# Optimization experiments

Measured on AMD Instinct MI355X. Metric: run time of the kernel, lower is better.

The kernel has to match this reference:

```python
import jax, jax.numpy as jnp
import numpy as np

B, S, E, H, V, O = 64, 512, 128, 1024, 128, 128


def setup_inputs() -> dict:
    key = jax.random.key(0)
    ks = jax.random.split(key, 16)
    nrm = lambda k, shp, s=0.05: s * jax.random.normal(k, shp, dtype=jnp.float32)
    return {
        "inputs": jax.random.randint(ks[0], (B, S), 0, V),
        "carry": jnp.zeros((B, H), dtype=jnp.float32),
        "embedding": nrm(ks[1], (V, E), 0.1),
        # GRUCell params (flax convention: input denses 'ir','iz','in' have bias;
        # hidden denses 'hr','hz' no bias; 'hn' has bias)
        "Wir": nrm(ks[2], (E, H)), "bir": jnp.zeros((H,), jnp.float32),
        "Whr": nrm(ks[3], (H, H)),
        "Wiz": nrm(ks[4], (E, H)), "biz": jnp.zeros((H,), jnp.float32),
        "Whz": nrm(ks[5], (H, H)),
        "Win": nrm(ks[6], (E, H)), "bin_": jnp.zeros((H,), jnp.float32),
        "Whn": nrm(ks[7], (H, H)), "bhn": jnp.zeros((H,), jnp.float32),
        "Wh": nrm(ks[8], (H, H)), "bh": jnp.zeros((H,), jnp.float32),
        "Wo": nrm(ks[9], (H, O)), "bo": jnp.zeros((O,), jnp.float32),
    }


def reference(inputs, carry, embedding, Wir, bir, Whr, Wiz, biz, Whz,
              Win, bin_, Whn, bhn, Wh, bh, Wo, bo):
    # Embedding lookup: [B, S, E]
    embed = jnp.take(embedding, inputs, axis=0)

    # GRU scan over time (axis=1 of embed)
    def step(h, x):  # h: [B,H], x: [B,E]
        r = jax.nn.sigmoid(x @ Wir + bir + h @ Whr)
        z = jax.nn.sigmoid(x @ Wiz + biz + h @ Whz)
        n = jnp.tanh(x @ Win + bin_ + r * (h @ Whn + bhn))
        h_new = (1.0 - z) * n + z * h
        return h_new, h_new

    xs = jnp.swapaxes(embed, 0, 1)  # [S, B, E]
    carry_out, ys = jax.lax.scan(step, carry, xs)  # ys: [S, B, H]
    outputs = jnp.swapaxes(ys, 0, 1).reshape(-1, H)  # [B*S, H]

    hidden = outputs @ Wh + bh            # Dense hidden_size
    logits = hidden @ Wo + bo             # Dense output_size -> [B*S, O]
    return (carry_out, logits)
```

## Files before the change

kernel.cpp:

```cpp
#include <hip/hip_runtime.h>
#include <hip/hip_cooperative_groups.h>
#include <math.h>

namespace cg = cooperative_groups;

#define Bp 64
#define Sp 512
#define Ep 128
#define Hp 1024
#define Vp 128
#define Op 128

typedef short s8v __attribute__((ext_vector_type(8)));
typedef float f4v __attribute__((ext_vector_type(4)));

#define WS_XV   0
#define WS_WHI  (WS_XV + Vp*3*Hp)
#define WS_WLO  (WS_WHI + (3*Hp*Hp)/2)
#define WS_HHI  (WS_WLO + (3*Hp*Hp)/2)
#define WS_HLO  (WS_HHI + (2*Bp*Hp)/2)
#define WS_YS   (WS_HLO + (2*Bp*Hp)/2)
#define WS_BAR  (WS_YS + (size_t)Sp*Bp*Hp)
#define WS_FLOATS (WS_BAR + 4*256)

__device__ __forceinline__ unsigned short f2bf(float x) {
  union { float f; unsigned u; } v; v.f = x;
  unsigned r = v.u + 0x7fffu + ((v.u >> 16) & 1u);
  return (unsigned short)(r >> 16);
}
__device__ __forceinline__ float bf2f(unsigned short h) {
  union { unsigned u; float f; } v; v.u = ((unsigned)h) << 16;
  return v.f;
}

__device__ __forceinline__ s8v ald16(const unsigned short* p) {
  union { unsigned long long q[2]; s8v v; } u;
  const unsigned long long* qp = (const unsigned long long*)p;
  u.q[0] = __hip_atomic_load(qp,     __ATOMIC_RELAXED, __HIP_MEMORY_SCOPE_AGENT);
  u.q[1] = __hip_atomic_load(qp + 1, __ATOMIC_RELAXED, __HIP_MEMORY_SCOPE_AGENT);
  return u.v;
}
__device__ __forceinline__ void ast8(unsigned short* p, unsigned long long v) {
  __hip_atomic_store((unsigned long long*)p, v, __ATOMIC_RELAXED, __HIP_MEMORY_SCOPE_AGENT);
}

__global__ __launch_bounds__(256) void xv_kernel(
    const float* __restrict__ emb,
    const float* __restrict__ Wir, const float* __restrict__ bir,
    const float* __restrict__ Wiz, const float* __restrict__ biz,
    const float* __restrict__ Win, const float* __restrict__ bin_,
    float* __restrict__ XV) {
  int n = blockIdx.x * 256 + threadIdx.x;
  int v = blockIdx.y;
  int g = n >> 10;
  int j = n & (Hp - 1);
  const float* W = (g == 0) ? Wir : ((g == 1) ? Wiz : Win);
  const float* bias = (g == 0) ? bir : ((g == 1) ? biz : bin_);
  float acc = bias[j];
  const float* ev = emb + (size_t)v * Ep;
  for (int e = 0; e < Ep; ++e) acc += ev[e] * W[(size_t)e * Hp + j];
  XV[(size_t)v * (3 * Hp) + n] = acc;
}

__global__ void wpack_kernel(const float* __restrict__ Whr,
                             const float* __restrict__ Whz,
                             const float* __restrict__ Whn,
                             unsigned short* __restrict__ Whi,
                             unsigned short* __restrict__ Wlo) {
  __shared__ float tile[32][33];
  int g = blockIdx.z;
  const float* src = (g == 0) ? Whr : ((g == 1) ? Whz : Whn);
  int kb = blockIdx.x * 32;
  int jb32 = blockIdx.y * 32;
  int tx = threadIdx.x, ty = threadIdx.y;
  #pragma unroll
  for (int i = 0; i < 4; ++i)
    tile[ty + 8 * i][tx] = src[(size_t)(kb + ty + 8 * i) * Hp + (jb32 + tx)];
  __syncthreads();
  #pragma unroll
  for (int i = 0; i < 4; ++i) {
    int jl = ty + 8 * i;
    int j = jb32 + jl;
    int dstRow = ((j >> 4) * 3 + g) * 16 + (j & 15);
    float w = tile[tx][jl];
    unsigned short hi = f2bf(w);
    Whi[(size_t)dstRow * Hp + kb + tx] = hi;
    Wlo[(size_t)dstRow * Hp + kb + tx] = f2bf(w - bf2f(hi));
  }
}

__global__ void h0_kernel(const float* __restrict__ carry,
                          unsigned short* __restrict__ hhi,
                          unsigned short* __restrict__ hlo,
                          unsigned* __restrict__ bar) {
  int i = blockIdx.x * 256 + threadIdx.x;
  float h = carry[i];
  unsigned short hi = f2bf(h);
  hhi[i] = hi;
  hlo[i] = f2bf(h - bf2f(hi));
  if (i < 4 * 256) bar[i] = 0u;
}

__global__ __launch_bounds__(256, 1) void gru_scan(
    const float* __restrict__ carry,
    float* __restrict__ ys,
    const unsigned short* __restrict__ Whi,
    const unsigned short* __restrict__ Wlo,
    const float* __restrict__ XV,
    const int* __restrict__ toks,
    const float* __restrict__ bhn,
    unsigned short* hhi,
    unsigned short* hlo,
    unsigned* bar) {
  __shared__ float part[3 * 4 * 64 * 4];
  __shared__ unsigned short hst[2][16][16];

  const int tid = threadIdx.x;
  const int wv = tid >> 6, lane = tid & 63;
  const int mb = blockIdx.x & 3, jb = blockIdx.x >> 2;
  const int col = lane & 15, kq = lane >> 4;

  unsigned* ctr = bar + mb * 256;

  const int kbase = wv * 256 + kq * 8;
  const unsigned short* bhp[3];
  const unsigned short* blp[3];
  #pragma unroll
  for (int g = 0; g < 3; ++g) {
    const size_t rowoff = ((size_t)(jb * 3 + g) * 16 + col) * Hp + kbase;
    bhp[g] = Whi + rowoff;
    blp[g] = Wlo + rowoff;
  }

  const int erow = tid >> 4, ecol = tid & 15;
  const int eb = mb * 16 + erow;
  const int ej = jb * 16 + ecol;
  const int elane = (erow >> 2) * 16 + ecol;
  const int er = erow & 3;
  const float bhnv = bhn[ej];

  const size_t aBase = (size_t)(mb * 16 + col) * Hp + kbase;
  const size_t eOff = (size_t)eb * Hp + ej;

  float holdR = carry[eOff];
  int tok0 = toks[eb * Sp + 0];
  const float* xvp0 = XV + (size_t)tok0 * (3 * Hp) + ej;
  float xr = xvp0[0], xz = xvp0[Hp], xn = xvp0[2 * Hp];

  const int splane = tid >> 6;
  const int srow = (tid >> 2) & 15;
  const int squad = tid & 3;
  const size_t sOff = (size_t)(mb * 16 + srow) * Hp + jb * 16 + squad * 4;

  for (int t = 0; t < Sp; ++t) {
    const unsigned short* hhiR = hhi + (size_t)(t & 1) * (Bp * Hp);
    const unsigned short* hloR = hlo + (size_t)(t & 1) * (Bp * Hp);
    unsigned short* hhiW = hhi + (size_t)((t + 1) & 1) * (Bp * Hp);
    unsigned short* hloW = hlo + (size_t)((t + 1) & 1) * (Bp * Hp);

    s8v ah[8], al[8];
    #pragma unroll
    for (int c = 0; c < 8; ++c) {
      ah[c] = ald16(hhiR + aBase + (size_t)c * 32);
      al[c] = ald16(hloR + aBase + (size_t)c * 32);
    }

    float xrN, xzN, xnN;
    {
      int tN = (t + 1 < Sp) ? (t + 1) : t;
      int tokN = toks[eb * Sp + tN];
      const float* xvpN = XV + (size_t)tokN * (3 * Hp) + ej;
      xrN = xvpN[0];
      xzN = xvpN[Hp];
      xnN = xvpN[2 * Hp];
    }

    f4v ar = {0.f, 0.f, 0.f, 0.f}, az = {0.f, 0.f, 0.f, 0.f}, an = {0.f, 0.f, 0.f, 0.f};
    #pragma unroll
    for (int c = 0; c < 8; ++c) {
      s8v b0 = *(const s8v*)(bhp[0] + c * 32);
      s8v b1 = *(const s8v*)(bhp[1] + c * 32);
      s8v b2 = *(const s8v*)(bhp[2] + c * 32);
      s8v l0 = *(const s8v*)(blp[0] + c * 32);
      s8v l1 = *(const s8v*)(blp[1] + c * 32);
      s8v l2 = *(const s8v*)(blp[2] + c * 32);
      ar = __builtin_amdgcn_mfma_f32_16x16x32_bf16(ah[c], b0, ar, 0, 0, 0);
      az = __builtin_amdgcn_mfma_f32_16x16x32_bf16(ah[c], b1, az, 0, 0, 0);
      an = __builtin_amdgcn_mfma_f32_16x16x32_bf16(ah[c], b2, an, 0, 0, 0);
      ar = __builtin_amdgcn_mfma_f32_16x16x32_bf16(al[c], b0, ar, 0, 0, 0);
      az = __builtin_amdgcn_mfma_f32_16x16x32_bf16(al[c], b1, az, 0, 0, 0);
      an = __builtin_amdgcn_mfma_f32_16x16x32_bf16(al[c], b2, an, 0, 0, 0);
      ar = __builtin_amdgcn_mfma_f32_16x16x32_bf16(ah[c], l0, ar, 0, 0, 0);
      az = __builtin_amdgcn_mfma_f32_16x16x32_bf16(ah[c], l1, az, 0, 0, 0);
      an = __builtin_amdgcn_mfma_f32_16x16x32_bf16(ah[c], l2, an, 0, 0, 0);
    }

    *(f4v*)&part[((0 * 4 + wv) * 64 + lane) * 4] = ar;
    *(f4v*)&part[((1 * 4 + wv) * 64 + lane) * 4] = az;
    *(f4v*)&part[((2 * 4 + wv) * 64 + lane) * 4] = an;
    __syncthreads();

    float sr = 0.f, sz = 0.f, sn = 0.f;
    #pragma unroll
    for (int w = 0; w < 4; ++w) {
      sr += part[((0 * 4 + w) * 64 + elane) * 4 + er];
      sz += part[((1 * 4 + w) * 64 + elane) * 4 + er];
      sn += part[((2 * 4 + w) * 64 + elane) * 4 + er];
    }

    float rg = 1.f / (1.f + expf(-(sr + xr)));
    float zg = 1.f / (1.f + expf(-(sz + xz)));
    float ng = tanhf(xn + rg * (sn + bhnv));
    float hnew = (1.f - zg) * ng + zg * holdR;

    __builtin_nontemporal_store(hnew, ys + (size_t)t * (Bp * Hp) + eOff);
    unsigned short hi16 = f2bf(hnew);
    hst[0][erow][ecol] = hi16;
    hst[1][erow][ecol] = f2bf(hnew - bf2f(hi16));

    holdR = hnew;
    xr = xrN; xz = xzN; xn = xnN;

    __syncthreads();
    if (tid < 128) {
      unsigned long long v = *(const unsigned long long*)&hst[splane][srow][squad * 4];
      ast8((splane ? hloW : hhiW) + sOff, v);
    }

    __threadfence_block();
    __syncthreads();
    if (tid == 0) {
      __hip_atomic_fetch_add(ctr, 1u, __ATOMIC_RELAXED, __HIP_MEMORY_SCOPE_AGENT);
      unsigned target = 64u * (unsigned)(t + 1);
      while (__hip_atomic_load(ctr, __ATOMIC_RELAXED, __HIP_MEMORY_SCOPE_AGENT) < target)
        __builtin_amdgcn_s_sleep(2);
    }
    __syncthreads();
  }
}

__global__ __launch_bounds__(256) void dense_kernel(
    const float* __restrict__ ys,
    const float* __restrict__ Wh, const float* __restrict__ bh,
    const float* __restrict__ Wo, const float* __restrict__ bo,
    float* __restrict__ out) {
  __shared__ float hs[16][1032];
  __shared__ float hid[16][1032];
  int tid = threadIdx.x;
  int r0 = blockIdx.x * 16;
  int bq = r0 / Sp;
  int s0 = r0 % Sp;

  for (int i = tid; i < 16 * 256; i += 256) {
    int m = i >> 8;
    int f = i & 255;
    float4 v = ((const float4*)(ys + (size_t)(s0 + m) * (Bp * Hp) + (size_t)bq * Hp))[f];
    ((float4*)&hs[m][0])[f] = v;
  }
  __syncthreads();

  float4 acc[16];
  float4 bh4 = ((const float4*)bh)[tid];
  #pragma unroll
  for (int m = 0; m < 16; ++m) acc[m] = bh4;
  for (int k = 0; k < Hp; ++k) {
    float4 w = ((const float4*)(Wh + (size_t)k * Hp))[tid];
    #pragma unroll
    for (int m = 0; m < 16; ++m) {
      float hv = hs[m][k];
      acc[m].x += hv * w.x;
      acc[m].y += hv * w.y;
      acc[m].z += hv * w.z;
      acc[m].w += hv * w.w;
    }
  }
  #pragma unroll
  for (int m = 0; m < 16; ++m) ((float4*)&hid[m][0])[tid] = acc[m];
  __syncthreads();

  int o = tid & (Op - 1);
  int half = tid >> 7;
  float lacc[8];
  float bov = bo[o];
  #pragma unroll
  for (int mm = 0; mm < 8; ++mm) lacc[mm] = bov;
  for (int k = 0; k < Hp; ++k) {
    float wo = Wo[(size_t)k * Op + o];
    #pragma unroll
    for (int mm = 0; mm < 8; ++mm) lacc[mm] += hid[half * 8 + mm][k] * wo;
  }
  float* lo = out + (size_t)Bp * Hp;
  #pragma unroll
  for (int mm = 0; mm < 8; ++mm) {
    int r = r0 + half * 8 + mm;
    lo[(size_t)r * Op + o] = lacc[mm];
  }
}

__global__ void carry_kernel(const float* __restrict__ ys, float* __restrict__ out) {
  int i = blockIdx.x * 256 + threadIdx.x;
  out[i] = ys[(size_t)(Sp - 1) * (Bp * Hp) + i];
}

extern "C" void kernel_launch(void* const* d_in, const int* in_sizes, int n_in,
                              void* d_out, int out_size, void* d_ws, size_t ws_size,
                              hipStream_t stream) {
  const int*   toks = (const int*)  d_in[0];
  const float* carry= (const float*)d_in[1];
  const float* emb  = (const float*)d_in[2];
  const float* Wir  = (const float*)d_in[3];
  const float* bir  = (const float*)d_in[4];
  const float* Whr  = (const float*)d_in[5];
  const float* Wiz  = (const float*)d_in[6];
  const float* biz  = (const float*)d_in[7];
  const float* Whz  = (const float*)d_in[8];
  const float* Win  = (const float*)d_in[9];
  const float* bin_ = (const float*)d_in[10];
  const float* Whn  = (const float*)d_in[11];
  const float* bhn  = (const float*)d_in[12];
  const float* Wh   = (const float*)d_in[13];
  const float* bh   = (const float*)d_in[14];
  const float* Wo   = (const float*)d_in[15];
  const float* bo   = (const float*)d_in[16];
  float* out = (float*)d_out;

  if (ws_size < WS_FLOATS * sizeof(float)) return;

  float* ws = (float*)d_ws;
  float* XV = ws + WS_XV;
  unsigned short* WhiP = (unsigned short*)(ws + WS_WHI);
  unsigned short* WloP = (unsigned short*)(ws + WS_WLO);
  unsigned short* hhi  = (unsigned short*)(ws + WS_HHI);
  unsigned short* hlo  = (unsigned short*)(ws + WS_HLO);
  float* ys = ws + WS_YS;
  unsigned* bar = (unsigned*)(ws + WS_BAR);

  xv_kernel<<<dim3(12, Vp), 256, 0, stream>>>(emb, Wir, bir, Wiz, biz, Win, bin_, XV);
  wpack_kernel<<<dim3(Hp / 32, Hp / 32, 3), dim3(32, 8), 0, stream>>>(Whr, Whz, Whn, WhiP, WloP);
  h0_kernel<<<(Bp * Hp) / 256, 256, 0, stream>>>(carry, hhi, hlo, bar);

  {
    void* args[] = {(void*)&carry, (void*)&ys, (void*)&WhiP, (void*)&WloP,
                    (void*)&XV, (void*)&toks, (void*)&bhn,
                    (void*)&hhi, (void*)&hlo, (void*)&bar};
    hipLaunchCooperativeKernel((const void*)gru_scan, dim3(256), dim3(256),
                               args, 0, stream);
  }

  carry_kernel<<<(Bp * Hp) / 256, 256, 0, stream>>>(ys, out);
  dense_kernel<<<(Bp * Sp) / 16, 256, 0, stream>>>(ys, Wh, bh, Wo, bo, out);
}
```

Measured before the change: 5.478 ms.

## Store hidden history as bf16 and run dense layers on split-bf16 MFMA

The scan no longer writes an fp32 ys buffer. Its bf16 hi part of h is kept for every timestep and serves both as the scan's double buffer and as the dense layers' input. The dense projections move from scalar FP32 FMA loops to MFMA bf16 instructions, with weights pre-transposed into hi/lo bf16 pairs. This cuts global traffic for ys and speeds up the large Wh matmul. In exchange the dense input uses only the bf16 hi part of h, and the intermediate hidden layer is rounded to bf16, which lowers accuracy. The block-to-(mb,jb) mapping is also reordered.

```diff
diff --git a/kernel.cpp b/kernel.cpp
--- a/kernel.cpp
+++ b/kernel.cpp
@@ -10,17 +10,21 @@
 #define Hp 1024
 #define Vp 128
 #define Op 128
+#define BH (Bp * Hp)
 
 typedef short s8v __attribute__((ext_vector_type(8)));
 typedef float f4v __attribute__((ext_vector_type(4)));
 
-#define WS_XV   0
-#define WS_WHI  (WS_XV + Vp*3*Hp)
-#define WS_WLO  (WS_WHI + (3*Hp*Hp)/2)
-#define WS_HHI  (WS_WLO + (3*Hp*Hp)/2)
-#define WS_HLO  (WS_HHI + (2*Bp*Hp)/2)
-#define WS_YS   (WS_HLO + (2*Bp*Hp)/2)
-#define WS_BAR  (WS_YS + (size_t)Sp*Bp*Hp)
+#define WS_XV    0
+#define WS_WHI   (WS_XV + Vp*3*Hp)
+#define WS_WLO   (WS_WHI + (3*Hp*Hp)/2)
+#define WS_YSH   (WS_WLO + (3*Hp*Hp)/2)
+#define WS_HLOP  (WS_YSH + ((size_t)(Sp+1)*BH)/2)
+#define WS_WHBH  (WS_HLOP + (2*BH)/2)
+#define WS_WHBL  (WS_WHBH + (Hp*Hp)/2)
+#define WS_WOBH  (WS_WHBL + (Hp*Hp)/2)
+#define WS_WOBL  (WS_WOBH + (Op*Hp)/2)
+#define WS_BAR   (WS_WOBL + (Op*Hp)/2)
 #define WS_FLOATS (WS_BAR + 4*256)
 
 __device__ __forceinline__ unsigned short f2bf(float x) {
@@ -89,35 +93,54 @@
   }
 }
 
+__global__ void tsplit_kernel(const float* __restrict__ src, int K, int N,
+                              unsigned short* __restrict__ dhi,
+                              unsigned short* __restrict__ dlo) {
+  __shared__ float tile[32][33];
+  int kb = blockIdx.x * 32, nb = blockIdx.y * 32;
+  int tx = threadIdx.x, ty = threadIdx.y;
+  #pragma unroll
+  for (int i = 0; i < 4; ++i)
+    tile[ty + 8 * i][tx] = src[(size_t)(kb + ty + 8 * i) * N + nb + tx];
+  __syncthreads();
+  #pragma unroll
+  for (int i = 0; i < 4; ++i) {
+    int nl = ty + 8 * i;
+    float w = tile[tx][nl];
+    unsigned short hi = f2bf(w);
+    dhi[(size_t)(nb + nl) * K + kb + tx] = hi;
+    dlo[(size_t)(nb + nl) * K + kb + tx] = f2bf(w - bf2f(hi));
+  }
+}
+
 __global__ void h0_kernel(const float* __restrict__ carry,
-                          unsigned short* __restrict__ hhi,
-                          unsigned short* __restrict__ hlo,
+                          unsigned short* __restrict__ ysH,
+                          unsigned short* __restrict__ hloP,
                           unsigned* __restrict__ bar) {
   int i = blockIdx.x * 256 + threadIdx.x;
   float h = carry[i];
   unsigned short hi = f2bf(h);
-  hhi[i] = hi;
-  hlo[i] = f2bf(h - bf2f(hi));
+  ysH[i] = hi;
+  hloP[i] = f2bf(h - bf2f(hi));
   if (i < 4 * 256) bar[i] = 0u;
 }
 
 __global__ __launch_bounds__(256, 1) void gru_scan(
     const float* __restrict__ carry,
-    float* __restrict__ ys,
+    unsigned short* ysH,
     const unsigned short* __restrict__ Whi,
     const unsigned short* __restrict__ Wlo,
     const float* __restrict__ XV,
     const int* __restrict__ toks,
     const float* __restrict__ bhn,
-    unsigned short* hhi,
-    unsigned short* hlo,
+    unsigned short* hloP,
     unsigned* bar) {
   __shared__ float part[3 * 4 * 64 * 4];
   __shared__ unsigned short hst[2][16][16];
 
   const int tid = threadIdx.x;
   const int wv = tid >> 6, lane = tid & 63;
-  const int mb = blockIdx.x & 3, jb = blockIdx.x >> 2;
+  const int mb = blockIdx.x >> 6, jb = blockIdx.x & 63;
   const int col = lane & 15, kq = lane >> 4;
 
   unsigned* ctr = bar + mb * 256;
@@ -153,10 +176,10 @@
   const size_t sOff = (size_t)(mb * 16 + srow) * Hp + jb * 16 + squad * 4;
 
   for (int t = 0; t < Sp; ++t) {
-    const unsigned short* hhiR = hhi + (size_t)(t & 1) * (Bp * Hp);
-    const unsigned short* hloR = hlo + (size_t)(t & 1) * (Bp * Hp);
-    unsigned short* hhiW = hhi + (size_t)((t + 1) & 1) * (Bp * Hp);
-    unsigned short* hloW = hlo + (size_t)((t + 1) & 1) * (Bp * Hp);
+    const unsigned short* hhiR = ysH + (size_t)t * BH;
+    const unsigned short* hloR = hloP + (size_t)(t & 1) * BH;
+    unsigned short* hhiW = ysH + (size_t)(t + 1) * BH;
+    unsigned short* hloW = hloP + (size_t)((t + 1) & 1) * BH;
 
     s8v ah[8], al[8];
     #pragma unroll
@@ -213,7 +236,6 @@
     float ng = tanhf(xn + rg * (sn + bhnv));
     float hnew = (1.f - zg) * ng + zg * holdR;
 
-    __builtin_nontemporal_store(hnew, ys + (size_t)t * (Bp * Hp) + eOff);
     unsigned short hi16 = f2bf(hnew);
     hst[0][erow][ecol] = hi16;
     hst[1][erow][ecol] = f2bf(hnew - bf2f(hi16));
@@ -239,67 +261,91 @@
   }
 }
 
-__global__ __launch_bounds__(256) void dense_kernel(
-    const float* __restrict__ ys,
-    const float* __restrict__ Wh, const float* __restrict__ bh,
-    const float* __restrict__ Wo, const float* __restrict__ bo,
+__global__ __launch_bounds__(256, 1) void dense_kernel(
+    const unsigned short* __restrict__ ysH,
+    const unsigned short* __restrict__ WhbH, const unsigned short* __restrict__ WhbL,
+    const float* __restrict__ bh,
+    const unsigned short* __restrict__ WobH, const unsigned short* __restrict__ WobL,
+    const float* __restrict__ bo,
     float* __restrict__ out) {
-  __shared__ float hs[16][1032];
-  __shared__ float hid[16][1032];
-  int tid = threadIdx.x;
-  int r0 = blockIdx.x * 16;
-  int bq = r0 / Sp;
-  int s0 = r0 % Sp;
-
-  for (int i = tid; i < 16 * 256; i += 256) {
-    int m = i >> 8;
-    int f = i & 255;
-    float4 v = ((const float4*)(ys + (size_t)(s0 + m) * (Bp * Hp) + (size_t)bq * Hp))[f];
-    ((float4*)&hs[m][0])[f] = v;
+  __shared__ unsigned short aHi[32 * 16 * 4 * 8];
+  __shared__ unsigned short hidBf[32 * 16 * 4 * 8];
+
+  const int tid = threadIdx.x;
+  const int wv = tid >> 6, lane = tid & 63;
+  const int col = lane & 15, kq = lane >> 4;
+  const int r0 = blockIdx.x * 16;
+  const int bq = r0 / Sp, s0 = r0 % Sp;
+
+  for (int i = tid; i < 16 * 128; i += 256) {
+    int m = i >> 7, c8 = i & 127;
+    int kc = c8 >> 2, kqi = c8 & 3;
+    const uint4* src = (const uint4*)(ysH + ((size_t)(s0 + m + 1) * Bp + bq) * Hp) + c8;
+    *(uint4*)&aHi[((kc * 16 + m) * 4 + kqi) * 8] = *src;
   }
   __syncthreads();
 
-  float4 acc[16];
-  float4 bh4 = ((const float4*)bh)[tid];
-  #pragma unroll
-  for (int m = 0; m < 16; ++m) acc[m] = bh4;
-  for (int k = 0; k < Hp; ++k) {
-    float4 w = ((const float4*)(Wh + (size_t)k * Hp))[tid];
-    #pragma unroll
-    for (int m = 0; m < 16; ++m) {
-      float hv = hs[m][k];
-      acc[m].x += hv * w.x;
-      acc[m].y += hv * w.y;
-      acc[m].z += hv * w.z;
-      acc[m].w += hv * w.w;
-    }
-  }
-  #pragma unroll
-  for (int m = 0; m < 16; ++m) ((float4*)&hid[m][0])[tid] = acc[m];
+  f4v acc[16];
+  #pragma unroll
+  for (int nt = 0; nt < 16; ++nt) acc[nt] = (f4v){0.f, 0.f, 0.f, 0.f};
+  for (int kc = 0; kc < 32; ++kc) {
+    s8v a = *(const s8v*)&aHi[(kc * 64 + col * 4 + kq) * 8];
+    const size_t koff = (size_t)kc * 32 + kq * 8;
+    #pragma unroll
+    for (int nt = 0; nt < 16; ++nt) {
+      int n = wv * 256 + nt * 16 + col;
+      s8v bHi = *(const s8v*)(WhbH + (size_t)n * Hp + koff);
+      s8v bLo = *(const s8v*)(WhbL + (size_t)n * Hp + koff);
+      acc[nt] = __builtin_amdgcn_mfma_f32_16x16x32_bf16(a, bHi, acc[nt], 0, 0, 0);
+      acc[nt] = __builtin_amdgcn_mfma_f32_16x16x32_bf16(a, bLo, acc[nt], 0, 0, 0);
+    }
+  }
+  #pragma unroll
+  for (int nt = 0; nt < 16; ++nt) {
+    int n = wv * 256 + nt * 16 + col;
+    float bias = bh[n];
+    int kc = n >> 5, kqi = (n >> 3) & 3, ii = n & 7;
+    #pragma unroll
+    for (int r = 0; r < 4; ++r) {
+      int m = kq * 4 + r;
+      hidBf[((kc * 16 + m) * 4 + kqi) * 8 + ii] = f2bf(acc[nt][r] + bias);
+    }
+  }
   __syncthreads();
 
-  int o = tid & (Op - 1);
-  int half = tid >> 7;
-  float lacc[8];
-  float bov = bo[o];
-  #pragma unroll
-  for (int mm = 0; mm < 8; ++mm) lacc[mm] = bov;
-  for (int k = 0; k < Hp; ++k) {
-    float wo = Wo[(size_t)k * Op + o];
-    #pragma unroll
-    for (int mm = 0; mm < 8; ++mm) lacc[mm] += hid[half * 8 + mm][k] * wo;
+  f4v lacc[2];
+  lacc[0] = (f4v){0.f, 0.f, 0.f, 0.f};
+  lacc[1] = (f4v){0.f, 0.f, 0.f, 0.f};
+  for (int kc = 0; kc < 32; ++kc) {
+    s8v a = *(const s8v*)&hidBf[(kc * 64 + col * 4 + kq) * 8];
+    const size_t koff = (size_t)kc * 32 + kq * 8;
+    #pragma unroll
+    for (int ot = 0; ot < 2; ++ot) {
+      int o = (wv * 2 + ot) * 16 + col;
+      s8v bHi = *(const s8v*)(WobH + (size_t)o * Hp + koff);
+      s8v bLo = *(const s8v*)(WobL + (size_t)o * Hp + koff);
+      lacc[ot] = __builtin_amdgcn_mfma_f32_16x16x32_bf16(a, bHi, lacc[ot], 0, 0, 0);
+      lacc[ot] = __builtin_amdgcn_mfma_f32_16x16x32_bf16(a, bLo, lacc[ot], 0, 0, 0);
+    }
   }
   float* lo = out + (size_t)Bp * Hp;
   #pragma unroll
-  for (int mm = 0; mm < 8; ++mm) {
-    int r = r0 + half * 8 + mm;
-    lo[(size_t)r * Op + o] = lacc[mm];
-  }
-}
-
-__global__ void carry_kernel(const float* __restrict__ ys, float* __restrict__ out) {
+  for (int ot = 0; ot < 2; ++ot) {
+    int o = (wv * 2 + ot) * 16 + col;
+    float bias = bo[o];
+    #pragma unroll
+    for (int r = 0; r < 4; ++r) {
+      int m = kq * 4 + r;
+      lo[(size_t)(r0 + m) * Op + o] = lacc[ot][r] + bias;
+    }
+  }
+}
+
+__global__ void carry_kernel(const unsigned short* __restrict__ ysH,
+                             const unsigned short* __restrict__ hloP,
+                             float* __restrict__ out) {
   int i = blockIdx.x * 256 + threadIdx.x;
-  out[i] = ys[(size_t)(Sp - 1) * (Bp * Hp) + i];
+  out[i] = bf2f(ysH[(size_t)Sp * BH + i]) + bf2f(hloP[(size_t)(Sp & 1) * BH + i]);
 }
 
 extern "C" void kernel_launch(void* const* d_in, const int* in_sizes, int n_in,
@@ -330,23 +376,28 @@
   float* XV = ws + WS_XV;
   unsigned short* WhiP = (unsigned short*)(ws + WS_WHI);
   unsigned short* WloP = (unsigned short*)(ws + WS_WLO);
-  unsigned short* hhi  = (unsigned short*)(ws + WS_HHI);
-  unsigned short* hlo  = (unsigned short*)(ws + WS_HLO);
-  float* ys = ws + WS_YS;
+  unsigned short* ysH  = (unsigned short*)(ws + WS_YSH);
+  unsigned short* hloP = (unsigned short*)(ws + WS_HLOP);
+  unsigned short* WhbH = (unsigned short*)(ws + WS_WHBH);
+  unsigned short* WhbL = (unsigned short*)(ws + WS_WHBL);
+  unsigned short* WobH = (unsigned short*)(ws + WS_WOBH);
+  unsigned short* WobL = (unsigned short*)(ws + WS_WOBL);
   unsigned* bar = (unsigned*)(ws + WS_BAR);
 
   xv_kernel<<<dim3(12, Vp), 256, 0, stream>>>(emb, Wir, bir, Wiz, biz, Win, bin_, XV);
   wpack_kernel<<<dim3(Hp / 32, Hp / 32, 3), dim3(32, 8), 0, stream>>>(Whr, Whz, Whn, WhiP, WloP);
-  h0_kernel<<<(Bp * Hp) / 256, 256, 0, stream>>>(carry, hhi, hlo, bar);
+  tsplit_kernel<<<dim3(Hp / 32, Hp / 32), dim3(32, 8), 0, stream>>>(Wh, Hp, Hp, WhbH, WhbL);
+  tsplit_kernel<<<dim3(Hp / 32, Op / 32), dim3(32, 8), 0, stream>>>(Wo, Hp, Op, WobH, WobL);
+  h0_kernel<<<BH / 256, 256, 0, stream>>>(carry, ysH, hloP, bar);
 
   {
-    void* args[] = {(void*)&carry, (void*)&ys, (void*)&WhiP, (void*)&WloP,
+    void* args[] = {(void*)&carry, (void*)&ysH, (void*)&WhiP, (void*)&WloP,
                     (void*)&XV, (void*)&toks, (void*)&bhn,
-                    (void*)&hhi, (void*)&hlo, (void*)&bar};
+                    (void*)&hloP, (void*)&bar};
     hipLaunchCooperativeKernel((const void*)gru_scan, dim3(256), dim3(256),
                                args, 0, stream);
   }
 
-  carry_kernel<<<(Bp * Hp) / 256, 256, 0, stream>>>(ys, out);
-  dense_kernel<<<(Bp * Sp) / 16, 256, 0, stream>>>(ys, Wh, bh, Wo, bo, out);
-}
+  carry_kernel<<<BH / 256, 256, 0, stream>>>(ysH, hloP, out);
+  dense_kernel<<<(Bp * Sp) / 16, 256, 0, stream>>>(ysH, WhbH, WhbL, bh, WobH, WobL, bo, out);
+}
```

After: 4.516 ms. -17.6%, faster.
